# Kernel optimization log

Hardware: AMD Instinct MI355X
Metric: run time of the kernel (lower is better)

The kernel has to match this reference:

```python
import jax, jax.numpy as jnp
import numpy as np

B, C, H, W = 8, 192, 128, 128
NH, WS, PS = 6, 8, 8
HD = C // NH
SCALE = HD ** -0.5

def _rel_pos_log(ws):
    # log-spaced signed relative coordinates, [N, N, 2]
    coords = np.stack(np.meshgrid(np.arange(ws), np.arange(ws), indexing='ij'))
    cf = coords.reshape(2, -1)
    rp = (cf[:, :, None] - cf[:, None, :]).transpose(1, 2, 0).astype(np.float32)
    return jnp.asarray(np.sign(rp) * np.log1p(np.abs(rp)))

def setup_inputs() -> dict:
    key = jax.random.key(0)
    ks = jax.random.split(key, 8)
    s = 0.02
    return {
        'x': jax.random.normal(ks[0], (B, C, H, W), jnp.float32),
        'V_w': jax.random.normal(ks[1], (C, C), jnp.float32) * s,
        'V_b': jnp.zeros((C,), jnp.float32),
        'QK_w': jax.random.normal(ks[2], (2 * C, C), jnp.float32) * s,
        'QK_b': jnp.zeros((2 * C,), jnp.float32),
        'proj_w': jax.random.normal(ks[3], (C, C), jnp.float32) * s,
        'proj_b': jnp.zeros((C,), jnp.float32),
        'meta_w1': jax.random.normal(ks[4], (2, 256), jnp.float32) * s,
        'meta_b1': jnp.zeros((256,), jnp.float32),
        'meta_w2': jax.random.normal(ks[5], (256, NH), jnp.float32) * s,
        'meta_b2': jnp.zeros((NH,), jnp.float32),
    }

def reference(x, V_w, V_b, QK_w, QK_b, proj_w, proj_b, meta_w1, meta_b1, meta_w2, meta_b2):
    N = WS * WS
    # 1x1 convs for V and QK
    v = jnp.einsum('bchw,oc->bohw', x, V_w) + V_b[None, :, None, None]
    qk = jnp.einsum('bchw,oc->bohw', x, QK_w) + QK_b[None, :, None, None]
    qkv = jnp.concatenate([qk, v], axis=1)  # [B, 3C, H, W]
    # window partition -> [B * nW, N, 3C]
    t = qkv.transpose(0, 2, 3, 1).reshape(B, H // WS, WS, W // WS, WS, 3 * C)
    wins = t.transpose(0, 1, 3, 2, 4, 5).reshape(-1, N, 3 * C)
    B_ = wins.shape[0]
    qkv3 = wins.reshape(B_, N, 3, NH, HD).transpose(2, 0, 3, 1, 4)
    q, k, vv = qkv3[0] * SCALE, qkv3[1], qkv3[2]  # [B_, NH, N, HD]
    # FFT cross-modulation of q and k over the 8x8 window grid (c = N/64 = 1)
    cg = N // (PS * PS)
    qp = q.reshape(B_, NH, cg, PS, PS, HD).transpose(0, 1, 2, 5, 3, 4)
    kp = k.reshape(B_, NH, cg, PS, PS, HD).transpose(0, 1, 2, 5, 3, 4)
    o = jnp.fft.irfft2(jnp.fft.rfft2(qp) * jnp.fft.rfft2(kp), s=(PS, PS))
    o = o.transpose(0, 1, 2, 4, 5, 3).reshape(B_, NH, N, HD)
    # relative position bias from meta MLP on log-spaced coords
    rp = _rel_pos_log(WS)  # [N, N, 2]
    bias = jax.nn.relu(rp @ meta_w1 + meta_b1) @ meta_w2 + meta_b2  # [N, N, NH]
    bias = bias.transpose(2, 0, 1)  # [NH, N, N]
    attn = jnp.einsum('bhnd,bhmd->bhnm', o, vv) + bias[None]
    attn = jax.nn.softmax(attn, axis=-1)
    y = jnp.einsum('bhnm,bhmd->bhnd', attn, vv).transpose(0, 2, 1, 3).reshape(B_, N, C)
    # window reverse -> [B, C, H, W]
    y = y.reshape(B, H // WS, W // WS, WS, WS, C).transpose(0, 1, 3, 2, 4, 5).reshape(B, H, W, C)
    y = y.transpose(0, 3, 1, 2)
    return jnp.einsum('bchw,oc->bohw', y, proj_w) + proj_b[None, :, None, None]
```

## Files before the change

### kernel.cpp

```cpp
#include <hip/hip_runtime.h>

#define SCALEQ 0.17677669529663687f

typedef __bf16 bf16x8 __attribute__((ext_vector_type(8)));
typedef float f32x4 __attribute__((ext_vector_type(4)));
typedef float f32x2 __attribute__((ext_vector_type(2)));

__device__ __forceinline__ float bflo(unsigned int u) { return __uint_as_float(u << 16); }
__device__ __forceinline__ float bfhi(unsigned int u) { return __uint_as_float(u & 0xffff0000u); }
__device__ __forceinline__ f32x2 b2x2(unsigned int u) {
    f32x2 r; r[0] = bflo(u); r[1] = bfhi(u); return r;
}
__device__ __forceinline__ unsigned short f2b(float f) {
    unsigned int u = __float_as_uint(f);
    u += 0x7fffu + ((u >> 16) & 1u);
    return (unsigned short)(u >> 16);
}
__device__ __forceinline__ unsigned int pk2(float a, float b) {
    return (unsigned int)f2b(a) | ((unsigned int)f2b(b) << 16);
}

#define RA     0
#define RB     24576
#define RC     49152
#define BTOFF  73728
#define LDS_BYTES 79128

#define WS_WQKV_ELEMS 110592
#define WS_WP_OFF_EL  110592
#define WS_BT_OFF_B   294912

__device__ __forceinline__ bf16x8 ldsf(const char* p) {
    uint4 u = *(const uint4*)p;
    return __builtin_bit_cast(bf16x8, u);
}
__device__ __forceinline__ bf16x8 gldf(const unsigned short* p) {
    uint4 u = *(const uint4*)p;
    return __builtin_bit_cast(bf16x8, u);
}

__global__ void wprep_kernel(const float* __restrict__ QKw, const float* __restrict__ Vw,
                             const float* __restrict__ Pw, unsigned short* __restrict__ wsb) {
    int i = blockIdx.x * 256 + threadIdx.x;
    if (i >= 147456) return;
    if (i < WS_WQKV_ELEMS) {
        int r = i / 192, c = i - r * 192;
        float v = (r < 384) ? QKw[r * 192 + c] : Vw[(r - 384) * 192 + c];
        wsb[i] = f2b(v);
    } else {
        int j = i - WS_WQKV_ELEMS;
        wsb[WS_WP_OFF_EL + j] = f2b(Pw[j]);
    }
}

__global__ void bias_table_kernel(const float* __restrict__ Mw1, const float* __restrict__ Mb1,
                                  const float* __restrict__ Mw2, const float* __restrict__ Mb2,
                                  float* __restrict__ bias_out) {
    int t = blockIdx.x * 64 + threadIdx.x;
    if (t >= 225) return;
    int dyi = t / 15, dxi = t % 15;
    float dy = (float)(dyi - 7), dx = (float)(dxi - 7);
    float f0 = copysignf(log1pf(fabsf(dy)), dy);
    float f1 = copysignf(log1pf(fabsf(dx)), dx);
    float a0 = Mb2[0], a1 = Mb2[1], a2 = Mb2[2], a3 = Mb2[3], a4 = Mb2[4], a5 = Mb2[5];
    for (int u = 0; u < 256; ++u) {
        float hv = fmaxf(f0 * Mw1[u] + f1 * Mw1[256 + u] + Mb1[u], 0.0f);
        const float* w2 = Mw2 + u * 6;
        a0 = fmaf(hv, w2[0], a0); a1 = fmaf(hv, w2[1], a1);
        a2 = fmaf(hv, w2[2], a2); a3 = fmaf(hv, w2[3], a3);
        a4 = fmaf(hv, w2[4], a4); a5 = fmaf(hv, w2[5], a5);
    }
    float* bt = bias_out + t * 6;
    bt[0] = a0; bt[1] = a1; bt[2] = a2; bt[3] = a3; bt[4] = a4; bt[5] = a5;
}

__global__ __launch_bounds__(512, 4)
void fused_win_attn(const float* __restrict__ x,
                    const float* __restrict__ Vb, const float* __restrict__ QKb,
                    const float* __restrict__ Pb,
                    const unsigned short* __restrict__ wqkv,
                    const unsigned short* __restrict__ wp,
                    const float* __restrict__ bias_g,
                    float* __restrict__ out)
{
    extern __shared__ char smem[];
    const int t   = threadIdx.x;
    const int wv  = t >> 6;
    const int l15 = t & 15;
    const int l4  = (t >> 4) & 3;

    const int wid = ((blockIdx.x & 7) << 8) | (blockIdx.x >> 3);
    const int b   = wid >> 8;
    const int wy  = (wid >> 4) & 15;
    const int wx  = wid & 15;
    const int y0  = wy * 8, x0 = wx * 8;

    const f32x4 zz = {0.0f, 0.0f, 0.0f, 0.0f};

    {
        float* bt = (float*)(smem + BTOFF);
        for (int i = t; i < 1350; i += 512) bt[i] = bias_g[i];
    }

    {
        const float* xb = x + (size_t)b * 192 * 16384;
        #pragma unroll
        for (int i = 0; i < 6; ++i) {
            int idx = t + 512 * i;
            int c = idx >> 4, sub = idx & 15;
            int r = sub >> 1, hf = sub & 1;
            float4 v4 = *(const float4*)(xb + c * 16384 + (y0 + r) * 128 + x0 + hf * 4);
            int n0 = r * 8 + hf * 4;
            unsigned short sv[4] = {f2b(v4.x), f2b(v4.y), f2b(v4.z), f2b(v4.w)};
            #pragma unroll
            for (int e = 0; e < 4; ++e) {
                int n = n0 + e;
                *(unsigned short*)(smem + RA + ((n * 384 + c * 2) ^ ((n & 7) << 4))) = sv[e];
            }
        }
    }
    __syncthreads();

    const int wcol = wv & 3, wrow = wv >> 2;
    unsigned int vp[3][2][2];
    {
        bf16x8 afr[6][2];
        #pragma unroll
        for (int ks = 0; ks < 6; ++ks)
            #pragma unroll
            for (int mtl = 0; mtl < 2; ++mtl) {
                int row = (wrow * 2 + mtl) * 16 + l15;
                afr[ks][mtl] = ldsf(smem + RA + ((row * 384 + ks * 64 + l4 * 16) ^ ((row & 7) << 4)));
            }
        __syncthreads();

        auto gemm3 = [&](int obase, f32x4 acc[3][2]) {
            bf16x8 bw[3][6];
            #pragma unroll
            for (int j = 0; j < 3; ++j) {
                const unsigned short* wr = wqkv + (size_t)(obase + j * 16 + l15) * 192 + l4 * 8;
                #pragma unroll
                for (int ks = 0; ks < 6; ++ks) bw[j][ks] = gldf(wr + ks * 32);
            }
            #pragma unroll
            for (int j = 0; j < 3; ++j) { acc[j][0] = zz; acc[j][1] = zz; }
            #pragma unroll
            for (int ks = 0; ks < 6; ++ks)
                #pragma unroll
                for (int j = 0; j < 3; ++j)
                    #pragma unroll
                    for (int mtl = 0; mtl < 2; ++mtl)
                        acc[j][mtl] = __builtin_amdgcn_mfma_f32_16x16x32_bf16(afr[ks][mtl], bw[j][ks], acc[j][mtl], 0, 0, 0);
        };

        {
            f32x4 acc[3][2];
            gemm3(wcol * 48, acc);
            #pragma unroll
            for (int j = 0; j < 3; ++j) {
                int och = wcol * 48 + j * 16 + l15;
                float bv = QKb[och];
                #pragma unroll
                for (int mtl = 0; mtl < 2; ++mtl)
                    #pragma unroll
                    for (int rr = 0; rr < 4; ++rr) {
                        int tok = (wrow * 2 + mtl) * 16 + l4 * 4 + rr;
                        *(unsigned short*)(smem + RA + ((tok * 384 + och * 2) ^ ((tok & 7) << 4)))
                            = f2b((acc[j][mtl][rr] + bv) * SCALEQ);
                    }
            }
        }
        {
            f32x4 acc[3][2];
            gemm3(192 + wcol * 48, acc);
            #pragma unroll
            for (int j = 0; j < 3; ++j) {
                int ch = wcol * 48 + j * 16 + l15;
                float bv = QKb[192 + ch];
                #pragma unroll
                for (int mtl = 0; mtl < 2; ++mtl)
                    #pragma unroll
                    for (int rr = 0; rr < 4; ++rr) {
                        int tok = (wrow * 2 + mtl) * 16 + l4 * 4 + rr;
                        *(unsigned short*)(smem + RB + ((tok * 384 + ch * 2) ^ ((tok & 7) << 4)))
                            = f2b(acc[j][mtl][rr] + bv);
                    }
            }
        }
        {
            f32x4 acc[3][2];
            gemm3(384 + wcol * 48, acc);
            #pragma unroll
            for (int j = 0; j < 3; ++j) {
                int ch = wcol * 48 + j * 16 + l15;
                float bv = Vb[ch];
                #pragma unroll
                for (int mtl = 0; mtl < 2; ++mtl) {
                    vp[j][mtl][0] = pk2(acc[j][mtl][0] + bv, acc[j][mtl][1] + bv);
                    vp[j][mtl][1] = pk2(acc[j][mtl][2] + bv, acc[j][mtl][3] + bv);
                }
            }
        }
    }
    __syncthreads();

    if (t < 384) {
        const int rn = t / 48, cc = t % 48;
        const int c0b = cc * 8;
        f32x2 acc[8][2];
        #pragma unroll
        for (int cn = 0; cn < 8; ++cn) {
            acc[cn][0] = (f32x2){0.0f, 0.0f};
            acc[cn][1] = (f32x2){0.0f, 0.0f};
        }
        #pragma unroll
        for (int kh = 0; kh < 2; ++kh) {
            uint2 karr[32];
            #pragma unroll
            for (int m = 0; m < 32; ++m) {
                int row = kh * 32 + m;
                karr[m] = *(const uint2*)(smem + RB + ((row * 384 + c0b) ^ ((row & 7) << 4)));
            }
            #pragma unroll
            for (int mrl = 0; mrl < 4; ++mrl) {
                const int mr = kh * 4 + mrl;
                f32x2 kf[8][2];
                #pragma unroll
                for (int mc = 0; mc < 8; ++mc) {
                    uint2 kv = karr[mrl * 8 + mc];
                    kf[mc][0] = b2x2(kv.x); kf[mc][1] = b2x2(kv.y);
                }
                const int npr = (rn - mr) & 7;
                #pragma unroll
                for (int npc = 0; npc < 8; ++npc) {
                    int np = npr * 8 + npc;
                    uint2 qv = *(const uint2*)(smem + RA + ((np * 384 + c0b) ^ ((np & 7) << 4)));
                    f32x2 qf0 = b2x2(qv.x), qf1 = b2x2(qv.y);
                    #pragma unroll
                    for (int mc = 0; mc < 8; ++mc) {
                        int cn = (npc + mc) & 7;
                        acc[cn][0] = qf0 * kf[mc][0] + acc[cn][0];
                        acc[cn][1] = qf1 * kf[mc][1] + acc[cn][1];
                    }
                }
            }
        }
        #pragma unroll
        for (int cn = 0; cn < 8; ++cn) {
            int n = rn * 8 + cn;
            uint2 pk;
            pk.x = pk2(acc[cn][0][0], acc[cn][0][1]);
            pk.y = pk2(acc[cn][1][0], acc[cn][1][1]);
            *(uint2*)(smem + RC + ((n * 384 + c0b) ^ ((n & 7) << 4))) = pk;
        }
    }
    __syncthreads();

    {
        #pragma unroll
        for (int j = 0; j < 3; ++j) {
            int ch = wcol * 48 + j * 16 + l15;
            #pragma unroll
            for (int mtl = 0; mtl < 2; ++mtl)
                #pragma unroll
                for (int pp = 0; pp < 2; ++pp) {
                    unsigned int pk = vp[j][mtl][pp];
                    int tok0 = (wrow * 2 + mtl) * 16 + l4 * 4 + pp * 2;
                    *(unsigned int*)(smem + RB + ((ch * 128 + tok0 * 2) ^ ((ch & 7) << 4))) = pk;
                    *(unsigned short*)(smem + RA + ((tok0 * 384 + ch * 2) ^ ((tok0 & 7) << 4)))
                        = (unsigned short)(pk & 0xffffu);
                    *(unsigned short*)(smem + RA + (((tok0 + 1) * 384 + ch * 2) ^ (((tok0 + 1) & 7) << 4)))
                        = (unsigned short)(pk >> 16);
                }
        }
    }
    __syncthreads();

    unsigned int pv[3][4][2];
    {
        const float* bt = (const float*)(smem + BTOFF);
        #pragma unroll
        for (int i = 0; i < 3; ++i) {
            int u = wv * 3 + i;
            int h = u >> 2, nt = u & 3;
            int brow = nt * 16 + l15;
            bf16x8 ofr = ldsf(smem + RC + ((brow * 384 + h * 64 + l4 * 16) ^ ((brow & 7) << 4)));
            int n = nt * 16 + l15;
            int nr = n >> 3, nc = n & 7;
            float s[4][4];
            #pragma unroll
            for (int mt = 0; mt < 4; ++mt) {
                int arow = mt * 16 + l15;
                bf16x8 vfr = ldsf(smem + RA + ((arow * 384 + h * 64 + l4 * 16) ^ ((arow & 7) << 4)));
                f32x4 a = __builtin_amdgcn_mfma_f32_16x16x32_bf16(vfr, ofr, zz, 0, 0, 0);
                #pragma unroll
                for (int rr = 0; rr < 4; ++rr) {
                    int m = mt * 16 + l4 * 4 + rr;
                    int dy = nr - (m >> 3) + 7, dx = nc - (m & 7) + 7;
                    s[mt][rr] = a[rr] + bt[(dy * 15 + dx) * 6 + h];
                }
            }
            float m0 = s[0][0];
            #pragma unroll
            for (int mt = 0; mt < 4; ++mt)
                #pragma unroll
                for (int rr = 0; rr < 4; ++rr) m0 = fmaxf(m0, s[mt][rr]);
            m0 = fmaxf(m0, __shfl_xor(m0, 16));
            m0 = fmaxf(m0, __shfl_xor(m0, 32));
            float sm = 0.0f;
            #pragma unroll
            for (int mt = 0; mt < 4; ++mt)
                #pragma unroll
                for (int rr = 0; rr < 4; ++rr) {
                    float p = __expf(s[mt][rr] - m0);
                    s[mt][rr] = p; sm += p;
                }
            sm += __shfl_xor(sm, 16);
            sm += __shfl_xor(sm, 32);
            float inv = 1.0f / sm;
            #pragma unroll
            for (int mt = 0; mt < 4; ++mt) {
                pv[i][mt][0] = pk2(s[mt][0] * inv, s[mt][1] * inv);
                pv[i][mt][1] = pk2(s[mt][2] * inv, s[mt][3] * inv);
            }
        }
    }
    __syncthreads();

    {
        #pragma unroll
        for (int i = 0; i < 3; ++i) {
            int u = wv * 3 + i;
            int h = u >> 2, nt = u & 3;
            bf16x8 pafr[2];
            #pragma unroll
            for (int ks = 0; ks < 2; ++ks) {
                unsigned int au[4];
                #pragma unroll
                for (int p = 0; p < 4; ++p) {
                    int srcl4 = (2 * l4 + (p >> 1)) & 3;
                    int src = srcl4 * 16 + l15;
                    unsigned int v0 = (unsigned int)__shfl((int)pv[i][2 * ks][p & 1], src, 64);
                    unsigned int v1 = (unsigned int)__shfl((int)pv[i][2 * ks + 1][p & 1], src, 64);
                    au[p] = (l4 & 2) ? v1 : v0;
                }
                uint4 u4 = {au[0], au[1], au[2], au[3]};
                pafr[ks] = __builtin_bit_cast(bf16x8, u4);
            }
            f32x4 acc[2];
            acc[0] = zz; acc[1] = zz;
            #pragma unroll
            for (int dt = 0; dt < 2; ++dt)
                #pragma unroll
                for (int ks = 0; ks < 2; ++ks) {
                    int drow = h * 32 + dt * 16 + l15;
                    bf16x8 vtf = ldsf(smem + RB + ((drow * 128 + ks * 64 + l4 * 16) ^ ((drow & 7) << 4)));
                    acc[dt] = __builtin_amdgcn_mfma_f32_16x16x32_bf16(pafr[ks], vtf, acc[dt], 0, 0, 0);
                }
            #pragma unroll
            for (int dt = 0; dt < 2; ++dt)
                #pragma unroll
                for (int rr = 0; rr < 4; ++rr) {
                    int tok = nt * 16 + l4 * 4 + rr;
                    int ch  = h * 32 + dt * 16 + l15;
                    *(unsigned short*)(smem + RC + ((tok * 384 + ch * 2) ^ ((tok & 7) << 4))) = f2b(acc[dt][rr]);
                }
        }
    }
    __syncthreads();

    {
        const int wc = wv & 3, wr = wv >> 2;
        bf16x8 wfr[3][6];
        #pragma unroll
        for (int jt = 0; jt < 3; ++jt) {
            int oc = wc * 48 + jt * 16;
            const unsigned short* wr_ = wp + (size_t)(oc + l15) * 192 + l4 * 8;
            #pragma unroll
            for (int ks = 0; ks < 6; ++ks) wfr[jt][ks] = gldf(wr_ + ks * 32);
        }
        f32x4 acc[3][2];
        #pragma unroll
        for (int jt = 0; jt < 3; ++jt) { acc[jt][0] = zz; acc[jt][1] = zz; }

        #pragma unroll
        for (int ks = 0; ks < 6; ++ks) {
            bf16x8 bfr[2];
            #pragma unroll
            for (int ntl = 0; ntl < 2; ++ntl) {
                int tok = (wr * 2 + ntl) * 16 + l15;
                bfr[ntl] = ldsf(smem + RC + ((tok * 384 + ks * 64 + l4 * 16) ^ ((tok & 7) << 4)));
            }
            #pragma unroll
            for (int jt = 0; jt < 3; ++jt)
                #pragma unroll
                for (int ntl = 0; ntl < 2; ++ntl)
                    acc[jt][ntl] = __builtin_amdgcn_mfma_f32_16x16x32_bf16(wfr[jt][ks], bfr[ntl], acc[jt][ntl], 0, 0, 0);
        }
        #pragma unroll
        for (int jt = 0; jt < 3; ++jt)
            #pragma unroll
            for (int rr = 0; rr < 4; ++rr) {
                int oc = wc * 48 + jt * 16 + l4 * 4 + rr;
                float pb = Pb[oc];
                float* obase = out + (size_t)(b * 192 + oc) * 16384;
                #pragma unroll
                for (int ntl = 0; ntl < 2; ++ntl) {
                    int tok = (wr * 2 + ntl) * 16 + l15;
                    obase[(y0 + (tok >> 3)) * 128 + x0 + (tok & 7)] = acc[jt][ntl][rr] + pb;
                }
            }
    }
}

extern "C" void kernel_launch(void* const* d_in, const int* in_sizes, int n_in,
                              void* d_out, int out_size, void* d_ws, size_t ws_size,
                              hipStream_t stream) {
    const float* x   = (const float*)d_in[0];
    const float* Vw  = (const float*)d_in[1];
    const float* Vb  = (const float*)d_in[2];
    const float* QKw = (const float*)d_in[3];
    const float* QKb = (const float*)d_in[4];
    const float* Pw  = (const float*)d_in[5];
    const float* Pb  = (const float*)d_in[6];
    const float* Mw1 = (const float*)d_in[7];
    const float* Mb1 = (const float*)d_in[8];
    const float* Mw2 = (const float*)d_in[9];
    const float* Mb2 = (const float*)d_in[10];
    float* outp = (float*)d_out;

    unsigned short* wsb  = (unsigned short*)d_ws;
    float* biasw = (float*)((char*)d_ws + WS_BT_OFF_B);

    wprep_kernel<<<dim3(576), dim3(256), 0, stream>>>(QKw, Vw, Pw, wsb);
    bias_table_kernel<<<dim3(4), dim3(64), 0, stream>>>(Mw1, Mb1, Mw2, Mb2, biasw);

    (void)hipFuncSetAttribute((const void*)fused_win_attn,
                              hipFuncAttributeMaxDynamicSharedMemorySize, LDS_BYTES);
    fused_win_attn<<<dim3(2048), dim3(512), LDS_BYTES, stream>>>(
        x, Vb, QKb, Pb, wsb, wsb + WS_WP_OFF_EL, biasw, outp);
}
```

Measured before the change: 299.2 us.

## Expand bias to full per-head table, fold q scale into weights, use native bf16 casts

```diff
diff --git a/kernel.cpp b/kernel.cpp
--- a/kernel.cpp
+++ b/kernel.cpp
@@ -3,6 +3,7 @@
 #define SCALEQ 0.17677669529663687f
 
 typedef __bf16 bf16x8 __attribute__((ext_vector_type(8)));
+typedef __bf16 bf16x2 __attribute__((ext_vector_type(2)));
 typedef float f32x4 __attribute__((ext_vector_type(4)));
 typedef float f32x2 __attribute__((ext_vector_type(2)));
 
@@ -12,23 +13,21 @@
     f32x2 r; r[0] = bflo(u); r[1] = bfhi(u); return r;
 }
 __device__ __forceinline__ unsigned short f2b(float f) {
-    unsigned int u = __float_as_uint(f);
-    u += 0x7fffu + ((u >> 16) & 1u);
-    return (unsigned short)(u >> 16);
+    return __builtin_bit_cast(unsigned short, (__bf16)f);
 }
 __device__ __forceinline__ unsigned int pk2(float a, float b) {
-    return (unsigned int)f2b(a) | ((unsigned int)f2b(b) << 16);
+    bf16x2 v; v[0] = (__bf16)a; v[1] = (__bf16)b;
+    return __builtin_bit_cast(unsigned int, v);
 }
 
 #define RA     0
 #define RB     24576
 #define RC     49152
-#define BTOFF  73728
-#define LDS_BYTES 79128
+#define LDS_BYTES 73728
 
 #define WS_WQKV_ELEMS 110592
 #define WS_WP_OFF_EL  110592
-#define WS_BT_OFF_B   294912
+#define WS_B2_OFF_B   294912
 
 __device__ __forceinline__ bf16x8 ldsf(const char* p) {
     uint4 u = *(const uint4*)p;
@@ -46,6 +45,7 @@
     if (i < WS_WQKV_ELEMS) {
         int r = i / 192, c = i - r * 192;
         float v = (r < 384) ? QKw[r * 192 + c] : Vw[(r - 384) * 192 + c];
+        if (r < 192) v *= SCALEQ;
         wsb[i] = f2b(v);
     } else {
         int j = i - WS_WQKV_ELEMS;
@@ -53,25 +53,22 @@
     }
 }
 
-__global__ void bias_table_kernel(const float* __restrict__ Mw1, const float* __restrict__ Mb1,
-                                  const float* __restrict__ Mw2, const float* __restrict__ Mb2,
-                                  float* __restrict__ bias_out) {
-    int t = blockIdx.x * 64 + threadIdx.x;
-    if (t >= 225) return;
-    int dyi = t / 15, dxi = t % 15;
-    float dy = (float)(dyi - 7), dx = (float)(dxi - 7);
+__global__ void bias2_kernel(const float* __restrict__ Mw1, const float* __restrict__ Mb1,
+                             const float* __restrict__ Mw2, const float* __restrict__ Mb2,
+                             float* __restrict__ out) {
+    int i = blockIdx.x * 256 + threadIdx.x;
+    if (i >= 6 * 64 * 64) return;
+    int h = i >> 12, n = (i >> 6) & 63, m = i & 63;
+    float dy = (float)((n >> 3) - (m >> 3));
+    float dx = (float)((n & 7) - (m & 7));
     float f0 = copysignf(log1pf(fabsf(dy)), dy);
     float f1 = copysignf(log1pf(fabsf(dx)), dx);
-    float a0 = Mb2[0], a1 = Mb2[1], a2 = Mb2[2], a3 = Mb2[3], a4 = Mb2[4], a5 = Mb2[5];
+    float a = Mb2[h];
     for (int u = 0; u < 256; ++u) {
         float hv = fmaxf(f0 * Mw1[u] + f1 * Mw1[256 + u] + Mb1[u], 0.0f);
-        const float* w2 = Mw2 + u * 6;
-        a0 = fmaf(hv, w2[0], a0); a1 = fmaf(hv, w2[1], a1);
-        a2 = fmaf(hv, w2[2], a2); a3 = fmaf(hv, w2[3], a3);
-        a4 = fmaf(hv, w2[4], a4); a5 = fmaf(hv, w2[5], a5);
-    }
-    float* bt = bias_out + t * 6;
-    bt[0] = a0; bt[1] = a1; bt[2] = a2; bt[3] = a3; bt[4] = a4; bt[5] = a5;
+        a = fmaf(hv, Mw2[u * 6 + h], a);
+    }
+    out[i] = a;
 }
 
 __global__ __launch_bounds__(512, 4)
@@ -80,7 +77,7 @@
                     const float* __restrict__ Pb,
                     const unsigned short* __restrict__ wqkv,
                     const unsigned short* __restrict__ wp,
-                    const float* __restrict__ bias_g,
+                    const float* __restrict__ bias2,
                     float* __restrict__ out)
 {
     extern __shared__ char smem[];
@@ -98,11 +95,6 @@
     const f32x4 zz = {0.0f, 0.0f, 0.0f, 0.0f};
 
     {
-        float* bt = (float*)(smem + BTOFF);
-        for (int i = t; i < 1350; i += 512) bt[i] = bias_g[i];
-    }
-
-    {
         const float* xb = x + (size_t)b * 192 * 16384;
         #pragma unroll
         for (int i = 0; i < 6; ++i) {
@@ -159,14 +151,14 @@
             #pragma unroll
             for (int j = 0; j < 3; ++j) {
                 int och = wcol * 48 + j * 16 + l15;
-                float bv = QKb[och];
+                float bv = QKb[och] * SCALEQ;
                 #pragma unroll
                 for (int mtl = 0; mtl < 2; ++mtl)
                     #pragma unroll
                     for (int rr = 0; rr < 4; ++rr) {
                         int tok = (wrow * 2 + mtl) * 16 + l4 * 4 + rr;
                         *(unsigned short*)(smem + RA + ((tok * 384 + och * 2) ^ ((tok & 7) << 4)))
-                            = f2b((acc[j][mtl][rr] + bv) * SCALEQ);
+                            = f2b(acc[j][mtl][rr] + bv);
                     }
             }
         }
@@ -278,7 +270,6 @@
 
     unsigned int pv[3][4][2];
     {
-        const float* bt = (const float*)(smem + BTOFF);
         #pragma unroll
         for (int i = 0; i < 3; ++i) {
             int u = wv * 3 + i;
@@ -286,19 +277,16 @@
             int brow = nt * 16 + l15;
             bf16x8 ofr = ldsf(smem + RC + ((brow * 384 + h * 64 + l4 * 16) ^ ((brow & 7) << 4)));
             int n = nt * 16 + l15;
-            int nr = n >> 3, nc = n & 7;
+            const float* bp = bias2 + ((h * 64 + n) << 6) + l4 * 4;
             float s[4][4];
             #pragma unroll
             for (int mt = 0; mt < 4; ++mt) {
                 int arow = mt * 16 + l15;
                 bf16x8 vfr = ldsf(smem + RA + ((arow * 384 + h * 64 + l4 * 16) ^ ((arow & 7) << 4)));
                 f32x4 a = __builtin_amdgcn_mfma_f32_16x16x32_bf16(vfr, ofr, zz, 0, 0, 0);
-                #pragma unroll
-                for (int rr = 0; rr < 4; ++rr) {
-                    int m = mt * 16 + l4 * 4 + rr;
-                    int dy = nr - (m >> 3) + 7, dx = nc - (m & 7) + 7;
-                    s[mt][rr] = a[rr] + bt[(dy * 15 + dx) * 6 + h];
-                }
+                float4 bb = *(const float4*)(bp + mt * 16);
+                s[mt][0] = a[0] + bb.x; s[mt][1] = a[1] + bb.y;
+                s[mt][2] = a[2] + bb.z; s[mt][3] = a[3] + bb.w;
             }
             float m0 = s[0][0];
             #pragma unroll
@@ -407,7 +395,8 @@
                 #pragma unroll
                 for (int ntl = 0; ntl < 2; ++ntl) {
                     int tok = (wr * 2 + ntl) * 16 + l15;
-                    obase[(y0 + (tok >> 3)) * 128 + x0 + (tok & 7)] = acc[jt][ntl][rr] + pb;
+                    __builtin_nontemporal_store(acc[jt][ntl][rr] + pb,
+                        obase + (y0 + (tok >> 3)) * 128 + x0 + (tok & 7));
                 }
             }
     }
@@ -429,14 +418,14 @@
     const float* Mb2 = (const float*)d_in[10];
     float* outp = (float*)d_out;
 
-    unsigned short* wsb  = (unsigned short*)d_ws;
-    float* biasw = (float*)((char*)d_ws + WS_BT_OFF_B);
+    unsigned short* wsb = (unsigned short*)d_ws;
+    float* b2 = (float*)((char*)d_ws + WS_B2_OFF_B);
 
     wprep_kernel<<<dim3(576), dim3(256), 0, stream>>>(QKw, Vw, Pw, wsb);
-    bias_table_kernel<<<dim3(4), dim3(64), 0, stream>>>(Mw1, Mb1, Mw2, Mb2, biasw);
+    bias2_kernel<<<dim3(96), dim3(256), 0, stream>>>(Mw1, Mb1, Mw2, Mb2, b2);
 
     (void)hipFuncSetAttribute((const void*)fused_win_attn,
                               hipFuncAttributeMaxDynamicSharedMemorySize, LDS_BYTES);
     fused_win_attn<<<dim3(2048), dim3(512), LDS_BYTES, stream>>>(
-        x, Vb, QKb, Pb, wsb, wsb + WS_WP_OFF_EL, biasw, outp);
-}
+        x, Vb, QKb, Pb, wsb, wsb + WS_WP_OFF_EL, b2, outp);
+}
```

Measured after the change: 307.2 us. 2.7% more time.
